# Kernel tuning notes

Hardware: AMD Instinct MI355X
Metric: run time of the kernel (lower is better)

The kernel has to match this reference:

```python
import jax, jax.numpy as jnp
import numpy as np

N_NODES = 100000
N_EDGES = 1600000
N_GRAPHS = 128
DIM = 128
N_LAYERS = 4
EPS = 1e-5


def setup_inputs() -> dict:
    key = jax.random.key(0)
    ks = jax.random.split(key, 8)
    h = jax.random.normal(ks[0], (N_NODES, DIM), dtype=jnp.float32)
    src = jax.random.randint(ks[1], (N_EDGES,), 0, N_NODES, dtype=jnp.int32)
    dst = jax.random.randint(ks[2], (N_EDGES,), 0, N_NODES, dtype=jnp.int32)
    graph_id = jnp.sort(jax.random.randint(ks[3], (N_NODES,), 0, N_GRAPHS, dtype=jnp.int32))
    sc = 1.0 / np.sqrt(DIM)
    W_embed = jax.random.normal(ks[4], (DIM, DIM), dtype=jnp.float32) * sc
    b_embed = jnp.zeros((DIM,), jnp.float32)
    W_layers = jax.random.normal(ks[5], (N_LAYERS, DIM, DIM), dtype=jnp.float32) * sc
    b_layers = jnp.zeros((N_LAYERS, DIM), jnp.float32)
    gamma = jnp.ones((N_LAYERS, DIM), jnp.float32)
    beta = jnp.zeros((N_LAYERS, DIM), jnp.float32)
    return {"h": h, "src": src, "dst": dst, "graph_id": graph_id,
            "W_embed": W_embed, "b_embed": b_embed, "W_layers": W_layers,
            "b_layers": b_layers, "gamma": gamma, "beta": beta}


def _gcn_forward(h, src, dst, graph_id, W_embed, b_embed, W_layers, b_layers, gamma, beta):
    # symmetric GraphConv normalization (norm='both'): D_out^{-1/2} on src, D_in^{-1/2} on dst
    ones_e = jnp.ones((src.shape[0],), h.dtype)
    deg_out = jax.ops.segment_sum(ones_e, src, num_segments=N_NODES)
    deg_in = jax.ops.segment_sum(ones_e, dst, num_segments=N_NODES)
    norm_src = jax.lax.rsqrt(jnp.maximum(deg_out, 1.0))
    norm_dst = jax.lax.rsqrt(jnp.maximum(deg_in, 1.0))

    # input embedding (dropout = identity in eval)
    h = h @ W_embed + b_embed

    for l in range(N_LAYERS):
        h_in = h
        # gather-aggregate-scatter: m_e = h_src * norm_src; sum into dst; scale by norm_dst
        m = (h * norm_src[:, None])[src]                         # [E, D]
        agg = jax.ops.segment_sum(m, dst, num_segments=N_NODES)  # [N, D]
        hl = (agg * norm_dst[:, None]) @ W_layers[l] + b_layers[l]
        # batch norm over node dimension (training-mode batch stats)
        mu = jnp.mean(hl, axis=0)
        var = jnp.var(hl, axis=0)
        hl = (hl - mu) * jax.lax.rsqrt(var + EPS) * gamma[l] + beta[l]
        hl = jax.nn.relu(hl)
        h = hl + h_in  # residual (dims match all layers)

    # mean readout per graph
    sums = jax.ops.segment_sum(h, graph_id, num_segments=N_GRAPHS)           # [G, D]
    cnts = jax.ops.segment_sum(jnp.ones((N_NODES,), h.dtype), graph_id, num_segments=N_GRAPHS)
    return sums / jnp.maximum(cnts, 1.0)[:, None]


def reference(h, src, dst, graph_id, W_embed, b_embed, W_layers, b_layers, gamma, beta):
    return _gcn_forward(h, src, dst, graph_id, W_embed, b_embed, W_layers, b_layers, gamma, beta)
```

## Files before the change

### kernel.cpp

```cpp
#include <hip/hip_runtime.h>
#include <hip/hip_bf16.h>
#include <hip/hip_fp16.h>


#define N_NODES 100000
#define N_EDGES 1600000
#define N_GRAPHS 128
#define DIM 128
#define N_LAYERS 4
#define BN_EPS 1e-5f
#define NBUCK 196
#define EPB 6250
#define SREP 64

typedef __attribute__((ext_vector_type(8))) _Float16 half8;
typedef __attribute__((ext_vector_type(4))) float floatx4;
typedef __attribute__((ext_vector_type(2))) float floatx2;

__global__ __launch_bounds__(256) void binA_k(const int* __restrict__ src,
                                              const int* __restrict__ dst,
                                              int* __restrict__ cnt_d,
                                              int* __restrict__ cnt_s,
                                              int* __restrict__ bh_d,
                                              int* __restrict__ bh_s) {
  __shared__ int hd[NBUCK], hs[NBUCK];
  int t = threadIdx.x;
  for (int i = t; i < NBUCK; i += 256) { hd[i] = 0; hs[i] = 0; }
  __syncthreads();
  int e0 = blockIdx.x * EPB;
  for (int e = e0 + t; e < e0 + EPB; e += 256) {
    atomicAdd(&hd[dst[e] >> 9], 1);
    atomicAdd(&hs[src[e] >> 9], 1);
  }
  __syncthreads();
  for (int i = t; i < NBUCK; i += 256) {
    int v = hd[i], v2 = hs[i];
    bh_d[blockIdx.x * NBUCK + i] = v;
    bh_s[blockIdx.x * NBUCK + i] = v2;
    if (v) atomicAdd(&cnt_d[i], v);
    if (v2) atomicAdd(&cnt_s[i], v2);
  }
}

__global__ __launch_bounds__(256) void scan196_k(
    const int* __restrict__ cnt_d, const int* __restrict__ cnt_s,
    int* __restrict__ base_d, int* __restrict__ cur_d,
    int* __restrict__ base_s, int* __restrict__ cur_s,
    int* __restrict__ row_start) {
  __shared__ int sd[256], ss[256];
  int t = threadIdx.x;
  int vd = (t < NBUCK) ? cnt_d[t] : 0;
  int vs = (t < NBUCK) ? cnt_s[t] : 0;
  sd[t] = vd;
  ss[t] = vs;
  __syncthreads();
  for (int off = 1; off < 256; off <<= 1) {
    int ad = (t >= off) ? sd[t - off] : 0;
    int as = (t >= off) ? ss[t - off] : 0;
    __syncthreads();
    sd[t] += ad;
    ss[t] += as;
    __syncthreads();
  }
  if (t < NBUCK) {
    base_d[t] = sd[t] - vd;
    cur_d[t] = sd[t] - vd;
    base_s[t] = ss[t] - vs;
    cur_s[t] = ss[t] - vs;
  }
  if (t == 0) {
    base_d[NBUCK] = N_EDGES;
    base_s[NBUCK] = N_EDGES;
    row_start[N_NODES] = N_EDGES;
  }
}

__global__ __launch_bounds__(256) void scat_k(
    const int* __restrict__ src, const int* __restrict__ dst,
    int* __restrict__ cur_d, int* __restrict__ cur_s,
    const int* __restrict__ bh_d, const int* __restrict__ bh_s,
    int* __restrict__ packed, unsigned short* __restrict__ locs) {
  __shared__ int hd[NBUCK], hs[NBUCK];
  int t = threadIdx.x;
  for (int i = t; i < NBUCK; i += 256) {
    hd[i] = bh_d[blockIdx.x * NBUCK + i];
    hs[i] = bh_s[blockIdx.x * NBUCK + i];
  }
  __syncthreads();
  if (t < NBUCK) {
    hd[t] = atomicAdd(&cur_d[t], hd[t]);
    hs[t] = atomicAdd(&cur_s[t], hs[t]);
  }
  __syncthreads();
  int e0 = blockIdx.x * EPB;
  for (int e = e0 + t; e < e0 + EPB; e += 256) {
    int s = src[e], d = dst[e];
    int slot = atomicAdd(&hd[d >> 9], 1);
    packed[slot] = ((d & 511) << 17) | s;
    int slot2 = atomicAdd(&hs[s >> 9], 1);
    locs[slot2] = (unsigned short)(s & 511);
  }
}

__global__ __launch_bounds__(256) void cd_k(const int* __restrict__ base_d,
                                            const int* __restrict__ packed,
                                            int* __restrict__ row_start,
                                            int* __restrict__ csr_src,
                                            float* __restrict__ norm_dst) {
  __shared__ int sdeg[512], sinc[512], scur[512];
  int t = threadIdx.x;
  int b = blockIdx.x;
  int nbase = b << 9;
  int e0 = base_d[b], e1 = base_d[b + 1];
  sdeg[t] = 0;
  sdeg[t + 256] = 0;
  __syncthreads();
  for (int e = e0 + t; e < e1; e += 256) atomicAdd(&sdeg[packed[e] >> 17], 1);
  __syncthreads();
  sinc[t] = sdeg[t];
  sinc[t + 256] = sdeg[t + 256];
  __syncthreads();
  for (int off = 1; off < 512; off <<= 1) {
    int a0 = (t >= off) ? sinc[t - off] : 0;
    int i1 = t + 256;
    int a1 = (i1 >= off) ? sinc[i1 - off] : 0;
    __syncthreads();
    sinc[t] += a0;
    sinc[i1] += a1;
    __syncthreads();
  }
#pragma unroll
  for (int half = 0; half < 2; ++half) {
    int j = t + half * 256;
    int lofs = e0 + sinc[j] - sdeg[j];
    scur[j] = lofs;
    int node = nbase + j;
    if (node < N_NODES) {
      row_start[node] = lofs;
      int d = sdeg[j];
      norm_dst[node] = rsqrtf((float)(d > 1 ? d : 1));
    }
  }
  __syncthreads();
  for (int e = e0 + t; e < e1; e += 256) {
    int p = packed[e];
    int slot = atomicAdd(&scur[p >> 17], 1);
    csr_src[slot] = p & 0x1FFFF;
  }
}

__global__ __launch_bounds__(256) void cs_k(const int* __restrict__ base_s,
                                            const unsigned short* __restrict__ locs,
                                            float* __restrict__ norm_src) {
  __shared__ int sdeg[512];
  int t = threadIdx.x;
  int b = blockIdx.x;
  int nbase = b << 9;
  int e0 = base_s[b], e1 = base_s[b + 1];
  sdeg[t] = 0;
  sdeg[t + 256] = 0;
  __syncthreads();
  for (int e = e0 + t; e < e1; e += 256) atomicAdd(&sdeg[locs[e]], 1);
  __syncthreads();
#pragma unroll
  for (int half = 0; half < 2; ++half) {
    int j = t + half * 256;
    int node = nbase + j;
    if (node < N_NODES) {
      int d = sdeg[j];
      norm_src[node] = rsqrtf((float)(d > 1 ? d : 1));
    }
  }
}

__global__ __launch_bounds__(256) void wswz_k(const float* __restrict__ W_embed,
                                              const float* __restrict__ W_layers,
                                              __half* __restrict__ Bsw) {
  int m = blockIdx.x >> 3, ct = blockIdx.x & 7;
  const float* Wm =
      (m == 0) ? W_embed : (W_layers + (size_t)(m - 1) * 16384);
  int ks = threadIdx.x >> 6, lane = threadIdx.x & 63;
  int n = ct * 16 + (lane & 15);
  int k0 = ks * 32 + (lane >> 4) * 8;
  __half* o = Bsw + ((((size_t)m * 8 + ct) * 4 + ks) * 64 + lane) * 8;
#pragma unroll
  for (int j = 0; j < 8; ++j) o[j] = __float2half(Wm[(k0 + j) * 128 + n]);
}

__device__ inline void mfma_core16(const __half* sA,
                                   const __half* __restrict__ Bsw,
                                   floatx4 (&acc)[8], int w, int lane,
                                   int quad, int lrow) {
#pragma unroll
  for (int ct = 0; ct < 8; ++ct) acc[ct] = (floatx4)(0.f);
#pragma unroll
  for (int ks = 0; ks < 4; ++ks) {
    int m = w * 16 + lrow;
    half8 afrag = *(const half8*)(&sA[m * 136 + ks * 32 + quad * 8]);
#pragma unroll
    for (int ct = 0; ct < 8; ++ct) {
      half8 bfrag = *(const half8*)(&Bsw[(((size_t)ct * 4 + ks) * 64 + lane) * 8]);
      acc[ct] = __builtin_amdgcn_mfma_f32_16x16x32_f16(afrag, bfrag, acc[ct],
                                                       0, 0, 0);
    }
  }
}

__global__ __launch_bounds__(256) void mfma_gemm_f32in(
    const float* __restrict__ X32, const __half* __restrict__ Bsw,
    const float* __restrict__ bias, __half* __restrict__ A16,
    unsigned char* __restrict__ S8, const float* __restrict__ norm_src) {
  __shared__ __half sA[64 * 136];
  const int tid = threadIdx.x;
  const int w = tid >> 6, lane = tid & 63;
  const int quad = lane >> 4, lrow = lane & 15;
  const int row_base = blockIdx.x * 64;

#pragma unroll
  for (int i = 0; i < 8; ++i) {
    int g = i * 256 + tid;
    int r = g >> 5, q = g & 31;
    int row = row_base + r;
    float4 v = make_float4(0.f, 0.f, 0.f, 0.f);
    if (row < N_NODES) v = ((const float4*)X32)[(size_t)row * 32 + q];
    union { __half2 h[2]; float f[2]; } u;
    u.h[0] = __floats2half2_rn(v.x, v.y);
    u.h[1] = __floats2half2_rn(v.z, v.w);
    *(float2*)(&sA[r * 136 + q * 4]) = *(float2*)u.f;
  }
  __syncthreads();

  floatx4 acc[8];
  mfma_core16(sA, Bsw, acc, w, lane, quad, lrow);

#pragma unroll
  for (int ct = 0; ct < 8; ++ct) {
    int col = ct * 16 + lrow;
    float b = bias[col];
#pragma unroll
    for (int reg = 0; reg < 4; ++reg) {
      int row = row_base + w * 16 + quad * 4 + reg;
      if (row < N_NODES) {
        float y = acc[ct][reg] + b;
        A16[(size_t)row * 128 + col] = __float2half(y);
        unsigned pb =
            __builtin_amdgcn_cvt_pk_fp8_f32(y * norm_src[row], 0.f, 0, false);
        S8[(size_t)row * 128 + col] = (unsigned char)(pb & 0xFF);
      }
    }
  }
}

__global__ __launch_bounds__(256) void mfma_gemm_f16(
    const __half* __restrict__ X16, const __half* __restrict__ Bsw,
    const float* __restrict__ bias, __half* __restrict__ hl16,
    float* __restrict__ stats) {
  __shared__ __half sA[64 * 136];
  const int tid = threadIdx.x;
  const int w = tid >> 6, lane = tid & 63;
  const int quad = lane >> 4, lrow = lane & 15;
  const int row_base = blockIdx.x * 64;

#pragma unroll
  for (int i = 0; i < 4; ++i) {
    int g = i * 256 + tid;
    int r = g >> 4, p = g & 15;
    int row = row_base + r;
    float4 v = make_float4(0.f, 0.f, 0.f, 0.f);
    if (row < N_NODES) v = ((const float4*)X16)[(size_t)row * 16 + p];
    *(float4*)(&sA[r * 136 + p * 8]) = v;
  }
  __syncthreads();

  floatx4 acc[8];
  mfma_core16(sA, Bsw, acc, w, lane, quad, lrow);

  float psum[8], pqsum[8];
#pragma unroll
  for (int ct = 0; ct < 8; ++ct) {
    int col = ct * 16 + lrow;
    float b = bias[col];
    psum[ct] = 0.f;
    pqsum[ct] = 0.f;
#pragma unroll
    for (int reg = 0; reg < 4; ++reg) {
      int row = row_base + w * 16 + quad * 4 + reg;
      if (row < N_NODES) {
        float y = acc[ct][reg] + b;
        hl16[(size_t)row * 128 + col] = __float2half(y);
        psum[ct] += y;
        pqsum[ct] += y * y;
      }
    }
  }

#pragma unroll
  for (int ct = 0; ct < 8; ++ct) {
    psum[ct] += __shfl_xor(psum[ct], 16, 64);
    psum[ct] += __shfl_xor(psum[ct], 32, 64);
    pqsum[ct] += __shfl_xor(pqsum[ct], 16, 64);
    pqsum[ct] += __shfl_xor(pqsum[ct], 32, 64);
  }
  __syncthreads();
  float* sred = (float*)sA;
  if (quad == 0) {
#pragma unroll
    for (int ct = 0; ct < 8; ++ct) {
      sred[w * 128 + ct * 16 + lrow] = psum[ct];
      sred[512 + w * 128 + ct * 16 + lrow] = pqsum[ct];
    }
  }
  __syncthreads();
  if (tid < 128) {
    float s = sred[tid] + sred[128 + tid] + sred[256 + tid] + sred[384 + tid];
    float q = sred[512 + tid] + sred[640 + tid] + sred[768 + tid] +
              sred[896 + tid];
    float* st = stats + (size_t)(blockIdx.x & (SREP - 1)) * 256;
    atomicAdd(&st[tid], s);
    atomicAdd(&st[128 + tid], q);
  }
}

__global__ __launch_bounds__(128) void bn_fin_k(const float* __restrict__ stats,
                                                const float* __restrict__ gamma,
                                                const float* __restrict__ beta,
                                                float* __restrict__ sc_sh) {
  int c = threadIdx.x;
  float s = 0.f, q = 0.f;
  for (int r = 0; r < SREP; ++r) {
    s += stats[r * 256 + c];
    q += stats[r * 256 + 128 + c];
  }
  const float invn = 1.0f / (float)N_NODES;
  float mean = s * invn;
  float var = q * invn - mean * mean;
  var = fmaxf(var, 0.f);
  float sc = gamma[c] * rsqrtf(var + BN_EPS);
  sc_sh[c] = sc;
  sc_sh[128 + c] = beta[c] - mean * sc;
}

__global__ __launch_bounds__(256) void bnrelu_k(
    const __half* __restrict__ hl16, __half* __restrict__ A16,
    unsigned char* __restrict__ S8, const float* __restrict__ sc_sh,
    const float* __restrict__ norm_src, int write_scaled) {
  int idx = blockIdx.x * 256 + threadIdx.x;
  int node = idx >> 4;
  int c8 = idx & 15;
  float4 hv4 = *(const float4*)(hl16 + (size_t)idx * 8);
  float4 av4 = *(const float4*)(A16 + (size_t)idx * 8);
  const __half2* hp = (const __half2*)&hv4;
  const __half2* ap = (const __half2*)&av4;
  const float4* sv = (const float4*)sc_sh;
  float4 s0 = sv[c8 * 2], s1 = sv[c8 * 2 + 1];
  float4 b0 = sv[32 + c8 * 2], b1 = sv[32 + c8 * 2 + 1];
  float n = write_scaled ? norm_src[node] : 0.f;
  float2 f0 = __half22float2(hp[0]), f1 = __half22float2(hp[1]);
  float2 f2 = __half22float2(hp[2]), f3 = __half22float2(hp[3]);
  float2 a0 = __half22float2(ap[0]), a1 = __half22float2(ap[1]);
  float2 a2 = __half22float2(ap[2]), a3 = __half22float2(ap[3]);
  float v[8];
  v[0] = fmaxf(f0.x * s0.x + b0.x, 0.f) + a0.x;
  v[1] = fmaxf(f0.y * s0.y + b0.y, 0.f) + a0.y;
  v[2] = fmaxf(f1.x * s0.z + b0.z, 0.f) + a1.x;
  v[3] = fmaxf(f1.y * s0.w + b0.w, 0.f) + a1.y;
  v[4] = fmaxf(f2.x * s1.x + b1.x, 0.f) + a2.x;
  v[5] = fmaxf(f2.y * s1.y + b1.y, 0.f) + a2.y;
  v[6] = fmaxf(f3.x * s1.z + b1.z, 0.f) + a3.x;
  v[7] = fmaxf(f3.y * s1.w + b1.w, 0.f) + a3.y;
  union { __half2 h[4]; float4 f; } ua;
#pragma unroll
  for (int q = 0; q < 4; ++q)
    ua.h[q] = __floats2half2_rn(v[2 * q], v[2 * q + 1]);
  *(float4*)(A16 + (size_t)idx * 8) = ua.f;
  if (write_scaled) {
    unsigned lo = 0, hi = 0;
    lo = __builtin_amdgcn_cvt_pk_fp8_f32(v[0] * n, v[1] * n, lo, false);
    lo = __builtin_amdgcn_cvt_pk_fp8_f32(v[2] * n, v[3] * n, lo, true);
    hi = __builtin_amdgcn_cvt_pk_fp8_f32(v[4] * n, v[5] * n, hi, false);
    hi = __builtin_amdgcn_cvt_pk_fp8_f32(v[6] * n, v[7] * n, hi, true);
    ((uint2*)S8)[idx] = make_uint2(lo, hi);
  }
}

__device__ inline void accf8x16(float (&a)[16], uint4 v) {
  floatx2 f;
  f = __builtin_amdgcn_cvt_pk_f32_fp8(v.x, false); a[0] += f.x;  a[1] += f.y;
  f = __builtin_amdgcn_cvt_pk_f32_fp8(v.x, true);  a[2] += f.x;  a[3] += f.y;
  f = __builtin_amdgcn_cvt_pk_f32_fp8(v.y, false); a[4] += f.x;  a[5] += f.y;
  f = __builtin_amdgcn_cvt_pk_f32_fp8(v.y, true);  a[6] += f.x;  a[7] += f.y;
  f = __builtin_amdgcn_cvt_pk_f32_fp8(v.z, false); a[8] += f.x;  a[9] += f.y;
  f = __builtin_amdgcn_cvt_pk_f32_fp8(v.z, true);  a[10] += f.x; a[11] += f.y;
  f = __builtin_amdgcn_cvt_pk_f32_fp8(v.w, false); a[12] += f.x; a[13] += f.y;
  f = __builtin_amdgcn_cvt_pk_f32_fp8(v.w, true);  a[14] += f.x; a[15] += f.y;
}

__global__ __launch_bounds__(256) void gather_k(
    const uint4* __restrict__ Hs, const int* __restrict__ row_start,
    const int* __restrict__ csr_src, const float* __restrict__ norm_dst,
    __half* __restrict__ out) {
  int node = (blockIdx.x * 256 + threadIdx.x) >> 3;
  int lane = threadIdx.x & 7;
  if (node >= N_NODES) return;
  int s0 = row_start[node], s1 = row_start[node + 1];
  float a[16];
#pragma unroll
  for (int i = 0; i < 16; ++i) a[i] = 0.f;
  for (int e = s0; e < s1; e += 8) {
    int cnt = s1 - e;
    if (cnt > 8) cnt = 8;
    int idx = (lane < cnt) ? csr_src[e + lane] : 0;
    int j = 0;
    for (; j + 4 <= cnt; j += 4) {
      uint4 v0 = Hs[(size_t)__shfl(idx, j, 8) * 8 + lane];
      uint4 v1 = Hs[(size_t)__shfl(idx, j + 1, 8) * 8 + lane];
      uint4 v2 = Hs[(size_t)__shfl(idx, j + 2, 8) * 8 + lane];
      uint4 v3 = Hs[(size_t)__shfl(idx, j + 3, 8) * 8 + lane];
      accf8x16(a, v0); accf8x16(a, v1); accf8x16(a, v2); accf8x16(a, v3);
    }
    for (; j < cnt; ++j) {
      accf8x16(a, Hs[(size_t)__shfl(idx, j, 8) * 8 + lane]);
    }
  }
  float nd = norm_dst[node];
  union { __half2 h[8]; float4 f[2]; } u;
#pragma unroll
  for (int q = 0; q < 8; ++q)
    u.h[q] = __floats2half2_rn(a[2 * q] * nd, a[2 * q + 1] * nd);
  float4* op = (float4*)(out + (size_t)node * 128 + lane * 16);
  op[0] = u.f[0];
  op[1] = u.f[1];
}

__global__ __launch_bounds__(256) void gbounds_k(const int* __restrict__ gid,
                                                 int* __restrict__ gstart) {
  int g = threadIdx.x;
  if (g > N_GRAPHS) return;
  int lo = 0, hi = N_NODES;
  while (lo < hi) {
    int mid = (lo + hi) >> 1;
    if (gid[mid] < g) lo = mid + 1; else hi = mid;
  }
  gstart[g] = lo;
}

__global__ __launch_bounds__(128) void gsum_k(const __half* __restrict__ A16,
                                              const int* __restrict__ gid,
                                              float* gsum) {
  int c = threadIdx.x;
  int n0 = blockIdx.x * 128;
  int n1 = n0 + 128;
  if (n1 > N_NODES) n1 = N_NODES;
  int cur = gid[n0];
  float local = 0.f;
  for (int n = n0; n < n1; ++n) {
    int g = gid[n];
    if (g != cur) {
      atomicAdd(&gsum[cur * 128 + c], local);
      local = 0.f;
      cur = g;
    }
    local += __half2float(A16[(size_t)n * 128 + c]);
  }
  atomicAdd(&gsum[cur * 128 + c], local);
}

__global__ __launch_bounds__(128) void gout_k(const float* __restrict__ gsum,
                                              const int* __restrict__ gstart,
                                              float* __restrict__ out) {
  int g = blockIdx.x, c = threadIdx.x;
  float cnt = (float)(gstart[g + 1] - gstart[g]);
  if (cnt < 1.f) cnt = 1.f;
  out[g * 128 + c] = gsum[g * 128 + c] / cnt;
}

extern "C" void kernel_launch(void* const* d_in, const int* in_sizes, int n_in,
                              void* d_out, int out_size, void* d_ws,
                              size_t ws_size, hipStream_t stream) {
  const float* h = (const float*)d_in[0];
  const int* src = (const int*)d_in[1];
  const int* dst = (const int*)d_in[2];
  const int* gid = (const int*)d_in[3];
  const float* W_embed = (const float*)d_in[4];
  const float* b_embed = (const float*)d_in[5];
  const float* W_layers = (const float*)d_in[6];
  const float* b_layers = (const float*)d_in[7];
  const float* gamma = (const float*)d_in[8];
  const float* beta = (const float*)d_in[9];
  float* out = (float*)d_out;
  (void)in_sizes; (void)n_in; (void)out_size; (void)ws_size;

  char* ws = (char*)d_ws;
  size_t o = 0;
  auto alloc = [&](size_t bytes) -> char* {
    char* p = ws + o;
    o = (o + bytes + 255) & ~(size_t)255;
    return p;
  };
  int* cnt_d = (int*)alloc(NBUCK * 4);
  int* cnt_s = (int*)alloc(NBUCK * 4);
  int* base_d = (int*)alloc((NBUCK + 1) * 4);
  int* cur_d = (int*)alloc(NBUCK * 4);
  int* base_s = (int*)alloc((NBUCK + 1) * 4);
  int* cur_s = (int*)alloc(NBUCK * 4);
  int* bh_d = (int*)alloc((size_t)256 * NBUCK * 4);
  int* bh_s = (int*)alloc((size_t)256 * NBUCK * 4);
  float* norm_src = (float*)alloc(N_NODES * 4);
  float* norm_dst = (float*)alloc(N_NODES * 4);
  int* row_start = (int*)alloc((N_NODES + 1) * 4);
  int* csr_src = (int*)alloc((size_t)N_EDGES * 4);
  int* packed = (int*)alloc((size_t)N_EDGES * 4);
  unsigned short* locs = (unsigned short*)alloc((size_t)N_EDGES * 2);
  float* stats4 = (float*)alloc((size_t)N_LAYERS * SREP * 256 * 4);
  float* gsum = (float*)alloc(N_GRAPHS * 128 * 4);
  int* gstart = (int*)alloc((N_GRAPHS + 1) * 4);
  float* sc_sh = (float*)alloc(256 * 4);
  __half* Bsw = (__half*)alloc(5 * 16384 * 2);
  __half* A16 = (__half*)alloc((size_t)N_NODES * 128 * 2);
  unsigned char* P0f8 = (unsigned char*)alloc((size_t)N_NODES * 128);
  __half* P1h = (__half*)alloc((size_t)N_NODES * 128 * 2);
  __half* H16 = (__half*)alloc((size_t)N_NODES * 128 * 2);

  hipMemsetAsync(cnt_d, 0, 2048, stream);
  hipMemsetAsync(stats4, 0, (size_t)N_LAYERS * SREP * 256 * 4 + 65536, stream);

  binA_k<<<256, 256, 0, stream>>>(src, dst, cnt_d, cnt_s, bh_d, bh_s);
  scan196_k<<<1, 256, 0, stream>>>(cnt_d, cnt_s, base_d, cur_d, base_s, cur_s,
                                   row_start);
  scat_k<<<256, 256, 0, stream>>>(src, dst, cur_d, cur_s, bh_d, bh_s, packed,
                                  locs);
  cd_k<<<NBUCK, 256, 0, stream>>>(base_d, packed, row_start, csr_src,
                                  norm_dst);
  cs_k<<<NBUCK, 256, 0, stream>>>(base_s, locs, norm_src);

  wswz_k<<<40, 256, 0, stream>>>(W_embed, W_layers, Bsw);

  mfma_gemm_f32in<<<(N_NODES + 63) / 64, 256, 0, stream>>>(
      h, Bsw, b_embed, A16, P0f8, norm_src);

  for (int l = 0; l < N_LAYERS; ++l) {
    float* stats = stats4 + (size_t)l * SREP * 256;
    gather_k<<<(N_NODES * 8 + 255) / 256, 256, 0, stream>>>(
        (const uint4*)P0f8, row_start, csr_src, norm_dst, P1h);
    mfma_gemm_f16<<<(N_NODES + 63) / 64, 256, 0, stream>>>(
        P1h, Bsw + (size_t)(1 + l) * 16384, b_layers + l * DIM, H16, stats);
    bn_fin_k<<<1, 128, 0, stream>>>(stats, gamma + l * DIM, beta + l * DIM,
                                    sc_sh);
    bnrelu_k<<<(N_NODES * 16 + 255) / 256, 256, 0, stream>>>(
        H16, A16, P0f8, sc_sh, norm_src, (l < N_LAYERS - 1) ? 1 : 0);
  }

  gbounds_k<<<1, 256, 0, stream>>>(gid, gstart);
  gsum_k<<<(N_NODES + 127) / 128, 128, 0, stream>>>(A16, gid, gsum);
  gout_k<<<N_GRAPHS, 128, 0, stream>>>(gsum, gstart, out);
}
```

Baseline: 575.2 us.

## Fuse edge gather into per-layer GEMM and stage GEMM outputs through LDS

Merges the per-layer fp8 gather-aggregate kernel into the MFMA GEMM kernel: each 64-row block gathers its neighbor sums straight into shared memory and then multiplies, removing the fp16 intermediate aggregate buffer and one launch per layer. GEMM epilogues in both the embed and layer kernels now stage accumulators through LDS in two halves so global stores are vectorized and row-contiguous instead of scattered 2-byte and 1-byte writes. The cost is lower gather parallelism per block (64 nodes per 256 threads in two passes, with the GEMM waiting on the slowest gather), plus extra syncs and shared memory.

```diff
diff --git a/kernel.cpp b/kernel.cpp
--- a/kernel.cpp
+++ b/kernel.cpp
@@ -206,6 +206,18 @@
   }
 }
 
+__device__ inline void accf8x16(float (&a)[16], uint4 v) {
+  floatx2 f;
+  f = __builtin_amdgcn_cvt_pk_f32_fp8(v.x, false); a[0] += f.x;  a[1] += f.y;
+  f = __builtin_amdgcn_cvt_pk_f32_fp8(v.x, true);  a[2] += f.x;  a[3] += f.y;
+  f = __builtin_amdgcn_cvt_pk_f32_fp8(v.y, false); a[4] += f.x;  a[5] += f.y;
+  f = __builtin_amdgcn_cvt_pk_f32_fp8(v.y, true);  a[6] += f.x;  a[7] += f.y;
+  f = __builtin_amdgcn_cvt_pk_f32_fp8(v.z, false); a[8] += f.x;  a[9] += f.y;
+  f = __builtin_amdgcn_cvt_pk_f32_fp8(v.z, true);  a[10] += f.x; a[11] += f.y;
+  f = __builtin_amdgcn_cvt_pk_f32_fp8(v.w, false); a[12] += f.x; a[13] += f.y;
+  f = __builtin_amdgcn_cvt_pk_f32_fp8(v.w, true);  a[14] += f.x; a[15] += f.y;
+}
+
 __global__ __launch_bounds__(256) void mfma_gemm_f32in(
     const float* __restrict__ X32, const __half* __restrict__ Bsw,
     const float* __restrict__ bias, __half* __restrict__ A16,
@@ -233,67 +245,115 @@
   floatx4 acc[8];
   mfma_core16(sA, Bsw, acc, w, lane, quad, lrow);
 
-#pragma unroll
-  for (int ct = 0; ct < 8; ++ct) {
-    int col = ct * 16 + lrow;
-    float b = bias[col];
-#pragma unroll
-    for (int reg = 0; reg < 4; ++reg) {
-      int row = row_base + w * 16 + quad * 4 + reg;
+  float bcol[8];
+#pragma unroll
+  for (int ct = 0; ct < 8; ++ct) bcol[ct] = bias[ct * 16 + lrow];
+
+  float* sC = (float*)sA;
+#pragma unroll
+  for (int h = 0; h < 2; ++h) {
+    __syncthreads();
+    if ((w >> 1) == h) {
+      int hw = w & 1;
+#pragma unroll
+      for (int ct = 0; ct < 8; ++ct)
+#pragma unroll
+        for (int reg = 0; reg < 4; ++reg)
+          sC[(hw * 16 + quad * 4 + reg) * 132 + ct * 16 + lrow] =
+              acc[ct][reg] + bcol[ct];
+    }
+    __syncthreads();
+#pragma unroll
+    for (int k = 0; k < 4; ++k) {
+      int c = k * 256 + tid;
+      int hr = c >> 5;
+      int col = (c & 31) * 4;
+      int row = row_base + h * 32 + hr;
       if (row < N_NODES) {
-        float y = acc[ct][reg] + b;
-        A16[(size_t)row * 128 + col] = __float2half(y);
-        unsigned pb =
-            __builtin_amdgcn_cvt_pk_fp8_f32(y * norm_src[row], 0.f, 0, false);
-        S8[(size_t)row * 128 + col] = (unsigned char)(pb & 0xFF);
+        float4 y = *(const float4*)&sC[hr * 132 + col];
+        union { __half2 hh[2]; float2 f; } u;
+        u.hh[0] = __floats2half2_rn(y.x, y.y);
+        u.hh[1] = __floats2half2_rn(y.z, y.w);
+        *(float2*)(A16 + (size_t)row * 128 + col) = u.f;
+        float ns = norm_src[row];
+        unsigned pb = 0;
+        pb = __builtin_amdgcn_cvt_pk_fp8_f32(y.x * ns, y.y * ns, pb, false);
+        pb = __builtin_amdgcn_cvt_pk_fp8_f32(y.z * ns, y.w * ns, pb, true);
+        *(unsigned*)(S8 + (size_t)row * 128 + col) = pb;
       }
     }
   }
 }
 
-__global__ __launch_bounds__(256) void mfma_gemm_f16(
-    const __half* __restrict__ X16, const __half* __restrict__ Bsw,
-    const float* __restrict__ bias, __half* __restrict__ hl16,
-    float* __restrict__ stats) {
+__global__ __launch_bounds__(256) void gag_k(
+    const uint4* __restrict__ Hs, const int* __restrict__ row_start,
+    const int* __restrict__ csr_src, const float* __restrict__ norm_dst,
+    const __half* __restrict__ Bsw, const float* __restrict__ bias,
+    __half* __restrict__ hl16, float* __restrict__ stats) {
   __shared__ __half sA[64 * 136];
+  __shared__ float sred[1024];
   const int tid = threadIdx.x;
   const int w = tid >> 6, lane = tid & 63;
   const int quad = lane >> 4, lrow = lane & 15;
   const int row_base = blockIdx.x * 64;
-
-#pragma unroll
-  for (int i = 0; i < 4; ++i) {
-    int g = i * 256 + tid;
-    int r = g >> 4, p = g & 15;
-    int row = row_base + r;
-    float4 v = make_float4(0.f, 0.f, 0.f, 0.f);
-    if (row < N_NODES) v = ((const float4*)X16)[(size_t)row * 16 + p];
-    *(float4*)(&sA[r * 136 + p * 8]) = v;
+  const int l8 = tid & 7;
+
+#pragma unroll
+  for (int pass = 0; pass < 2; ++pass) {
+    int r = pass * 32 + (tid >> 3);
+    int node = row_base + r;
+    float a[16];
+#pragma unroll
+    for (int i = 0; i < 16; ++i) a[i] = 0.f;
+    float nd = 0.f;
+    if (node < N_NODES) {
+      nd = norm_dst[node];
+      int s0 = row_start[node], s1 = row_start[node + 1];
+      for (int e = s0; e < s1; e += 8) {
+        int cnt = s1 - e;
+        if (cnt > 8) cnt = 8;
+        int idx = (l8 < cnt) ? csr_src[e + l8] : 0;
+        int j = 0;
+        for (; j + 4 <= cnt; j += 4) {
+          uint4 v0 = Hs[(size_t)__shfl(idx, j, 8) * 8 + l8];
+          uint4 v1 = Hs[(size_t)__shfl(idx, j + 1, 8) * 8 + l8];
+          uint4 v2 = Hs[(size_t)__shfl(idx, j + 2, 8) * 8 + l8];
+          uint4 v3 = Hs[(size_t)__shfl(idx, j + 3, 8) * 8 + l8];
+          accf8x16(a, v0); accf8x16(a, v1); accf8x16(a, v2); accf8x16(a, v3);
+        }
+        for (; j < cnt; ++j) {
+          accf8x16(a, Hs[(size_t)__shfl(idx, j, 8) * 8 + l8]);
+        }
+      }
+    }
+    union { __half2 hh[8]; float4 f[2]; } u;
+#pragma unroll
+    for (int q = 0; q < 8; ++q)
+      u.hh[q] = __floats2half2_rn(a[2 * q] * nd, a[2 * q + 1] * nd);
+    *(float4*)(&sA[r * 136 + l8 * 16]) = u.f[0];
+    *(float4*)(&sA[r * 136 + l8 * 16 + 8]) = u.f[1];
   }
   __syncthreads();
 
   floatx4 acc[8];
   mfma_core16(sA, Bsw, acc, w, lane, quad, lrow);
 
-  float psum[8], pqsum[8];
+  float bcol[8], psum[8], pqsum[8];
 #pragma unroll
   for (int ct = 0; ct < 8; ++ct) {
-    int col = ct * 16 + lrow;
-    float b = bias[col];
+    bcol[ct] = bias[ct * 16 + lrow];
     psum[ct] = 0.f;
     pqsum[ct] = 0.f;
 #pragma unroll
     for (int reg = 0; reg < 4; ++reg) {
       int row = row_base + w * 16 + quad * 4 + reg;
       if (row < N_NODES) {
-        float y = acc[ct][reg] + b;
-        hl16[(size_t)row * 128 + col] = __float2half(y);
+        float y = acc[ct][reg] + bcol[ct];
         psum[ct] += y;
         pqsum[ct] += y * y;
       }
     }
   }
-
 #pragma unroll
   for (int ct = 0; ct < 8; ++ct) {
     psum[ct] += __shfl_xor(psum[ct], 16, 64);
@@ -301,8 +361,6 @@
     pqsum[ct] += __shfl_xor(pqsum[ct], 16, 64);
     pqsum[ct] += __shfl_xor(pqsum[ct], 32, 64);
   }
-  __syncthreads();
-  float* sred = (float*)sA;
   if (quad == 0) {
 #pragma unroll
     for (int ct = 0; ct < 8; ++ct) {
@@ -318,6 +376,36 @@
     float* st = stats + (size_t)(blockIdx.x & (SREP - 1)) * 256;
     atomicAdd(&st[tid], s);
     atomicAdd(&st[128 + tid], q);
+  }
+
+  float* sC = (float*)sA;
+#pragma unroll
+  for (int h = 0; h < 2; ++h) {
+    __syncthreads();
+    if ((w >> 1) == h) {
+      int hw = w & 1;
+#pragma unroll
+      for (int ct = 0; ct < 8; ++ct)
+#pragma unroll
+        for (int reg = 0; reg < 4; ++reg)
+          sC[(hw * 16 + quad * 4 + reg) * 132 + ct * 16 + lrow] =
+              acc[ct][reg] + bcol[ct];
+    }
+    __syncthreads();
+#pragma unroll
+    for (int k = 0; k < 4; ++k) {
+      int c = k * 256 + tid;
+      int hr = c >> 5;
+      int col = (c & 31) * 4;
+      int row = row_base + h * 32 + hr;
+      if (row < N_NODES) {
+        float4 y = *(const float4*)&sC[hr * 132 + col];
+        union { __half2 hh[2]; float2 f; } u;
+        u.hh[0] = __floats2half2_rn(y.x, y.y);
+        u.hh[1] = __floats2half2_rn(y.z, y.w);
+        *(float2*)(hl16 + (size_t)row * 128 + col) = u.f;
+      }
+    }
   }
 }
 
@@ -383,55 +471,6 @@
   }
 }
 
-__device__ inline void accf8x16(float (&a)[16], uint4 v) {
-  floatx2 f;
-  f = __builtin_amdgcn_cvt_pk_f32_fp8(v.x, false); a[0] += f.x;  a[1] += f.y;
-  f = __builtin_amdgcn_cvt_pk_f32_fp8(v.x, true);  a[2] += f.x;  a[3] += f.y;
-  f = __builtin_amdgcn_cvt_pk_f32_fp8(v.y, false); a[4] += f.x;  a[5] += f.y;
-  f = __builtin_amdgcn_cvt_pk_f32_fp8(v.y, true);  a[6] += f.x;  a[7] += f.y;
-  f = __builtin_amdgcn_cvt_pk_f32_fp8(v.z, false); a[8] += f.x;  a[9] += f.y;
-  f = __builtin_amdgcn_cvt_pk_f32_fp8(v.z, true);  a[10] += f.x; a[11] += f.y;
-  f = __builtin_amdgcn_cvt_pk_f32_fp8(v.w, false); a[12] += f.x; a[13] += f.y;
-  f = __builtin_amdgcn_cvt_pk_f32_fp8(v.w, true);  a[14] += f.x; a[15] += f.y;
-}
-
-__global__ __launch_bounds__(256) void gather_k(
-    const uint4* __restrict__ Hs, const int* __restrict__ row_start,
-    const int* __restrict__ csr_src, const float* __restrict__ norm_dst,
-    __half* __restrict__ out) {
-  int node = (blockIdx.x * 256 + threadIdx.x) >> 3;
-  int lane = threadIdx.x & 7;
-  if (node >= N_NODES) return;
-  int s0 = row_start[node], s1 = row_start[node + 1];
-  float a[16];
-#pragma unroll
-  for (int i = 0; i < 16; ++i) a[i] = 0.f;
-  for (int e = s0; e < s1; e += 8) {
-    int cnt = s1 - e;
-    if (cnt > 8) cnt = 8;
-    int idx = (lane < cnt) ? csr_src[e + lane] : 0;
-    int j = 0;
-    for (; j + 4 <= cnt; j += 4) {
-      uint4 v0 = Hs[(size_t)__shfl(idx, j, 8) * 8 + lane];
-      uint4 v1 = Hs[(size_t)__shfl(idx, j + 1, 8) * 8 + lane];
-      uint4 v2 = Hs[(size_t)__shfl(idx, j + 2, 8) * 8 + lane];
-      uint4 v3 = Hs[(size_t)__shfl(idx, j + 3, 8) * 8 + lane];
-      accf8x16(a, v0); accf8x16(a, v1); accf8x16(a, v2); accf8x16(a, v3);
-    }
-    for (; j < cnt; ++j) {
-      accf8x16(a, Hs[(size_t)__shfl(idx, j, 8) * 8 + lane]);
-    }
-  }
-  float nd = norm_dst[node];
-  union { __half2 h[8]; float4 f[2]; } u;
-#pragma unroll
-  for (int q = 0; q < 8; ++q)
-    u.h[q] = __floats2half2_rn(a[2 * q] * nd, a[2 * q + 1] * nd);
-  float4* op = (float4*)(out + (size_t)node * 128 + lane * 16);
-  op[0] = u.f[0];
-  op[1] = u.f[1];
-}
-
 __global__ __launch_bounds__(256) void gbounds_k(const int* __restrict__ gid,
                                                  int* __restrict__ gstart) {
   int g = threadIdx.x;
@@ -518,7 +557,6 @@
   __half* Bsw = (__half*)alloc(5 * 16384 * 2);
   __half* A16 = (__half*)alloc((size_t)N_NODES * 128 * 2);
   unsigned char* P0f8 = (unsigned char*)alloc((size_t)N_NODES * 128);
-  __half* P1h = (__half*)alloc((size_t)N_NODES * 128 * 2);
   __half* H16 = (__half*)alloc((size_t)N_NODES * 128 * 2);
 
   hipMemsetAsync(cnt_d, 0, 2048, stream);
@@ -540,10 +578,9 @@
 
   for (int l = 0; l < N_LAYERS; ++l) {
     float* stats = stats4 + (size_t)l * SREP * 256;
-    gather_k<<<(N_NODES * 8 + 255) / 256, 256, 0, stream>>>(
-        (const uint4*)P0f8, row_start, csr_src, norm_dst, P1h);
-    mfma_gemm_f16<<<(N_NODES + 63) / 64, 256, 0, stream>>>(
-        P1h, Bsw + (size_t)(1 + l) * 16384, b_layers + l * DIM, H16, stats);
+    gag_k<<<(N_NODES + 63) / 64, 256, 0, stream>>>(
+        (const uint4*)P0f8, row_start, csr_src, norm_dst,
+        Bsw + (size_t)(1 + l) * 16384, b_layers + l * DIM, H16, stats);
     bn_fin_k<<<1, 128, 0, stream>>>(stats, gamma + l * DIM, beta + l * DIM,
                                     sc_sh);
     bnrelu_k<<<(N_NODES * 16 + 255) / 256, 256, 0, stream>>>(
```

Result: faster. 561.2 us (-2.4%).
